# Kernel optimization log

Hardware: AMD Instinct MI355X
Metric: run time of the kernel (lower is better)

The kernel has to match this reference:

```python
import jax, jax.numpy as jnp
import numpy as np

B, L, C = 2, 4096, 1024
H, WIN = 16, 128            # num_heads, window_size (each side)
D = C // H                  # head_dim = 64


def setup_inputs() -> dict:
    key = jax.random.key(0)
    ks = jax.random.split(key, 9)
    s = 0.02
    return {
        "x": jax.random.normal(ks[0], (B, L, C), jnp.float32),
        # Linear weights stored as [in, out] (y = x @ W + b), same math as torch Linear.
        "wq": jax.random.normal(ks[1], (C, C), jnp.float32) * s,
        "bq": jnp.zeros((C,), jnp.float32),
        "wk": jax.random.normal(ks[2], (C, C), jnp.float32) * s,
        "bk": jnp.zeros((C,), jnp.float32),
        "wv": jax.random.normal(ks[3], (C, C), jnp.float32) * s,
        "bv": jnp.zeros((C,), jnp.float32),
        "wo": jax.random.normal(ks[4], (C, C), jnp.float32) * s,
        "bo": jnp.zeros((C,), jnp.float32),
    }


def reference(x, wq, bq, wk, bk, wv, bv, wo, bo):
    b, l, c = x.shape
    nb = l // WIN

    def heads(t):  # (B,L,C) -> (B,H,L,D)
        return t.reshape(b, l, H, D).transpose(0, 2, 1, 3)

    q = heads(x @ wq + bq)
    k = heads(x @ wk + bk)
    v = heads(x @ wv + bv)

    # and ARE included in the softmax, exactly as the original module does).
    kp = jnp.pad(k, ((0, 0), (0, 0), (WIN, WIN), (0, 0)))
    vp = jnp.pad(v, ((0, 0), (0, 0), (WIN, WIN), (0, 0)))

    idx = np.arange(nb)[:, None] * WIN + np.arange(3 * WIN)[None, :]  # [nb, 3W]
    kb = kp[:, :, idx]  # [B,H,nb,3W,D]
    vb = vp[:, :, idx]  # [B,H,nb,3W,D]
    qb = q.reshape(b, H, nb, WIN, D)

    scores = jnp.einsum('bhnqd,bhnkd->bhnqk', qb, kb) / float(np.sqrt(D))
    r = np.arange(WIN)[:, None]
    col = np.arange(3 * WIN)[None, :]
    band = jnp.asarray(np.abs(col - r - WIN) <= WIN)
    scores = jnp.where(band, scores, -jnp.inf)
    probs = jax.nn.softmax(scores, axis=-1)

    out = jnp.einsum('bhnqk,bhnkd->bhnqd', probs, vb)
    out = out.reshape(b, H, l, D).transpose(0, 2, 1, 3).reshape(b, l, c)
    return out @ wo + bo
```

## Files before the change

kernel.cpp:

```cpp
#include <hip/hip_runtime.h>

using short8  = __attribute__((ext_vector_type(8))) short;
using short4v = __attribute__((ext_vector_type(4))) short;
using floatx4 = __attribute__((ext_vector_type(4))) float;

#define MFMA_B16(a, b, c) __builtin_amdgcn_mfma_f32_16x16x32_bf16(a, b, c, 0, 0, 0)

__device__ __forceinline__ short f2bf(float f) {
  union { float f; unsigned u; } v; v.f = f;
  unsigned r = v.u + 0x7fffu + ((v.u >> 16) & 1u);
  return (short)(r >> 16);
}
__device__ __forceinline__ short f2bf_rtz(float f) {
  union { float f; unsigned u; } v; v.f = f;
  return (short)(v.u >> 16);
}

__device__ __forceinline__ void gload_lds16(const short* g, short* l) {
  __builtin_amdgcn_global_load_lds(
      (const __attribute__((address_space(1))) unsigned int*)g,
      (__attribute__((address_space(3))) unsigned int*)l, 16, 0, 0);
}

__global__ __launch_bounds__(256) void prep(
    const float4* __restrict__ x, short4v* __restrict__ xb,
    const float* __restrict__ w0, const float* __restrict__ w1,
    const float* __restrict__ w2, const float* __restrict__ w3,
    short* __restrict__ wT) {
  __shared__ float tile[32][33];
  int blk = blockIdx.x;
  if (blk < 8192) {
    int i = blk * 256 + threadIdx.x;
    float4 v = x[i];
    short4v o = { f2bf(v.x), f2bf(v.y), f2bf(v.z), f2bf(v.w) };
    xb[i] = o;
  } else {
    int r = blk - 8192;
    int z = r >> 10; r &= 1023;
    const float* w = z == 0 ? w0 : (z == 1 ? w1 : (z == 2 ? w2 : w3));
    short* out = wT + (size_t)z * 1024 * 1024;
    int n0 = (r & 31) * 32, k0 = (r >> 5) * 32;
    int tx = threadIdx.x & 31, ty = threadIdx.x >> 5;
#pragma unroll
    for (int i = 0; i < 4; ++i)
      tile[ty + i * 8][tx] = w[(size_t)(k0 + ty + i * 8) * 1024 + n0 + tx];
    __syncthreads();
#pragma unroll
    for (int i = 0; i < 4; ++i)
      out[(size_t)(n0 + ty + i * 8) * 1024 + k0 + tx] = f2bf(tile[tx][ty + i * 8]);
  }
}

__global__ __launch_bounds__(512, 2) void gemm_qkv(
    const short* __restrict__ xb, const short* __restrict__ wT,
    const float* __restrict__ bq, const float* __restrict__ bk,
    const float* __restrict__ bv, short* __restrict__ qkv) {
  __shared__ __align__(16) short As[2 * 16384];
  __shared__ __align__(16) short Bs[2 * 3 * 8192];

  int bid = blockIdx.x;
  int xcd = bid & 7;
  int idx = bid >> 3;
  int mb  = xcd * 4 + (idx & 3);
  int nb  = idx >> 2;
  int m0 = mb * 256, n0 = nb * 128;

  const int tid = threadIdx.x;
  const int w = tid >> 6, lane = tid & 63, quad = lane >> 4, l16 = lane & 15;
  const int wm = w >> 2, wn = w & 3;
  const int srow = tid >> 3;
  const int scol = ((tid & 7) ^ (srow & 7)) * 8;

  floatx4 zf = {0.f, 0.f, 0.f, 0.f};
  floatx4 acc[3][8][2];
#pragma unroll
  for (int z = 0; z < 3; ++z)
#pragma unroll
    for (int i = 0; i < 8; ++i) { acc[z][i][0] = zf; acc[z][i][1] = zf; }

  const short* gA = xb + (size_t)(m0 + srow) * 1024 + scol;
  const short* gB0 = wT + (size_t)(n0 + srow) * 1024 + scol;

  auto stA = [&](int buf, int q, int kt) {
    gload_lds16(gA + (size_t)q * 64 * 1024 + kt * 64,
                As + buf * 16384 + q * 4096 + w * 512);
  };
  auto stB = [&](int buf, int z, int q, int kt) {
    gload_lds16(gB0 + (size_t)z * 1024 * 1024 + (size_t)q * 64 * 1024 + kt * 64,
                Bs + (buf * 3 + z) * 8192 + q * 4096 + w * 512);
  };

  short8 aF[8], bF[4];
  auto ldA = [&](int buf, int mh) {
    const char* base = (const char*)(As + buf * 16384);
#pragma unroll
    for (int m = 0; m < 4; ++m)
#pragma unroll
      for (int kk = 0; kk < 2; ++kk) {
        int row = wm * 128 + mh * 64 + m * 16 + l16;
        int off = row * 128 + kk * 64 + quad * 16;
        off ^= (row & 7) << 4;
        aF[m * 2 + kk] = *(const short8*)(base + off);
      }
  };
  auto ldB = [&](int buf, int z) {
    const char* base = (const char*)(Bs + (buf * 3 + z) * 8192);
#pragma unroll
    for (int n = 0; n < 2; ++n)
#pragma unroll
      for (int kk = 0; kk < 2; ++kk) {
        int row = wn * 32 + n * 16 + l16;
        int off = row * 128 + kk * 64 + quad * 16;
        off ^= (row & 7) << 4;
        bF[n * 2 + kk] = *(const short8*)(base + off);
      }
  };
  auto mm = [&](int z, int mh) {
#pragma unroll
    for (int m = 0; m < 4; ++m)
#pragma unroll
      for (int n = 0; n < 2; ++n)
#pragma unroll
        for (int kk = 0; kk < 2; ++kk)
          acc[z][mh * 4 + m][n] =
              MFMA_B16(aF[m * 2 + kk], bF[n * 2 + kk], acc[z][mh * 4 + m][n]);
  };

  stA(0, 0, 0); stA(0, 1, 0); stA(0, 2, 0); stA(0, 3, 0);
  stB(0, 0, 0, 0); stB(0, 0, 1, 0); stB(0, 1, 0, 0); stB(0, 1, 1, 0);
  stB(0, 2, 0, 0); stB(0, 2, 1, 0);
  stA(1, 0, 1); stA(1, 2, 1); stA(1, 1, 1); stA(1, 3, 1);
  stB(1, 0, 0, 1); stB(1, 0, 1, 1); stB(1, 1, 0, 1); stB(1, 1, 1, 1);
  asm volatile("s_waitcnt vmcnt(8)" ::: "memory");
  __builtin_amdgcn_s_barrier();

#pragma unroll 2
  for (int t = 0; t < 16; ++t) {
    const int cb = t & 1, nbuf = cb ^ 1;
    ldA(cb, 0);
    ldB(cb, 0);
    if (t + 1 < 16) { stB(nbuf, 2, 0, t + 1); stB(nbuf, 2, 1, t + 1); }
    __builtin_amdgcn_s_setprio(1); mm(0, 0); __builtin_amdgcn_s_setprio(0);
    __builtin_amdgcn_s_barrier();
    ldB(cb, 1);
    if (t + 2 < 16) { stA(cb, 0, t + 2); stA(cb, 2, t + 2); }
    __builtin_amdgcn_s_setprio(1); mm(1, 0); __builtin_amdgcn_s_setprio(0);
    __builtin_amdgcn_s_barrier();
    ldB(cb, 2);
    __builtin_amdgcn_s_setprio(1); mm(2, 0); __builtin_amdgcn_s_setprio(0);
    __builtin_amdgcn_s_barrier();
    ldA(cb, 1);
    ldB(cb, 0);
    __builtin_amdgcn_s_setprio(1); mm(0, 1); __builtin_amdgcn_s_setprio(0);
    __builtin_amdgcn_s_barrier();
    ldB(cb, 1);
    if (t + 2 < 16) {
      stA(cb, 1, t + 2); stA(cb, 3, t + 2);
      stB(cb, 0, 0, t + 2); stB(cb, 0, 1, t + 2);
    }
    __builtin_amdgcn_s_setprio(1); mm(1, 1); __builtin_amdgcn_s_setprio(0);
    __builtin_amdgcn_s_barrier();
    ldB(cb, 2);
    if (t + 2 < 16) { stB(cb, 1, 0, t + 2); stB(cb, 1, 1, t + 2); }
    __builtin_amdgcn_s_setprio(1); mm(2, 1); __builtin_amdgcn_s_setprio(0);
    if (t + 2 < 16) {
      asm volatile("s_waitcnt vmcnt(8)" ::: "memory");
    } else {
      asm volatile("s_waitcnt vmcnt(0)" ::: "memory");
    }
    __builtin_amdgcn_s_barrier();
  }

  const float* biases[3] = {bq, bk, bv};
#pragma unroll
  for (int z = 0; z < 3; ++z) {
    const float* bias = biases[z];
    short* out = qkv + (size_t)z * 8192 * 1024;
    float qs = (z == 0) ? 0.125f * 1.44269504f : 1.0f;
#pragma unroll
    for (int mf = 0; mf < 8; ++mf)
#pragma unroll
      for (int nf = 0; nf < 2; ++nf)
#pragma unroll
        for (int rg = 0; rg < 4; ++rg) {
          int m = m0 + wm * 128 + mf * 16 + quad * 4 + rg;
          int cc = n0 + wn * 32 + nf * 16 + l16;
          float v = (acc[z][mf][nf][rg] + bias[cc]) * qs;
          int b = m >> 12, l = m & 4095;
          int hh = cc >> 6, d = cc & 63;
          out[((size_t)(b * 16 + hh) * 4096 + l) * 64 + d] = f2bf(v);
        }
  }
}

__global__ __launch_bounds__(256) void attn_kern(const short* __restrict__ qkv,
                                                 short* __restrict__ attnb) {
  const int L = 4096, H = 16;
  int n = blockIdx.x, h = blockIdx.y, b = blockIdx.z;
  const size_t hs = (size_t)L * 64;
  const short* Qp = qkv + (size_t)(b * H + h) * hs;
  const short* Kp = qkv + (size_t)8192 * 1024 + (size_t)(b * H + h) * hs;
  const short* Vp = qkv + (size_t)2 * 8192 * 1024 + (size_t)(b * H + h) * hs;

  __shared__ __align__(16) short kt[128][72];
  __shared__ __align__(16) short vt[64][136];
  __shared__ __align__(16) short pl[4][32][136];

  int tid = threadIdx.x, w = tid >> 6, lane = tid & 63, quad = lane >> 4, l16 = lane & 15;

  short8 onesf;
  {
    short ov = (l16 == 0) ? (short)0x3F80 : (short)0;
#pragma unroll
    for (int j = 0; j < 8; ++j) onesf[j] = ov;
  }

  short8 qf[2][2];
#pragma unroll
  for (int rt = 0; rt < 2; ++rt)
#pragma unroll
    for (int ks = 0; ks < 2; ++ks)
      qf[rt][ks] = *(const short8*)(Qp + (size_t)(n * 128 + w * 32 + rt * 16 + l16) * 64 + ks * 32 + quad * 8);

  floatx4 zf = {0.f, 0.f, 0.f, 0.f};
  floatx4 o[2][4];
  floatx4 osum[2];
#pragma unroll
  for (int i = 0; i < 2; ++i) {
    osum[i] = zf;
#pragma unroll
    for (int j = 0; j < 4; ++j) o[i][j] = zf;
  }

#pragma unroll
  for (int c = 0; c < 3; ++c) {
    int bk = n - 1 + c;
    bool inr = (c == 1) || (c == 0 ? (n > 0) : (n < 31));
    __syncthreads();
    if (inr) {
      const short* kc_ = Kp + (size_t)bk * 128 * 64;
      int kr = tid >> 2, ksg = (tid & 3) * 16;
#pragma unroll
      for (int p = 0; p < 2; ++p) {
        int r2 = p * 64 + kr;
        *(short8*)(&kt[r2][ksg])     = *(const short8*)(kc_ + r2 * 64 + ksg);
        *(short8*)(&kt[r2][ksg + 8]) = *(const short8*)(kc_ + r2 * 64 + ksg + 8);
      }
      const short* vc_ = Vp + (size_t)bk * 128 * 64;
      int vkey = tid & 31, vsg = (tid >> 5) * 8;
#pragma unroll
      for (int p = 0; p < 4; ++p) {
        int r2 = p * 32 + vkey;
        short8 vv = *(const short8*)(vc_ + r2 * 64 + vsg);
#pragma unroll
        for (int j = 0; j < 8; ++j) vt[vsg + j][r2] = vv[j];
      }
    } else {
      short8 z8 = {0, 0, 0, 0, 0, 0, 0, 0};
      int kr = tid >> 2, ksg = (tid & 3) * 16;
#pragma unroll
      for (int p = 0; p < 2; ++p) {
        int r2 = p * 64 + kr;
        *(short8*)(&kt[r2][ksg])     = z8;
        *(short8*)(&kt[r2][ksg + 8]) = z8;
      }
      int vr = tid >> 2, vsg2 = (tid & 3) * 32;
#pragma unroll
      for (int q2 = 0; q2 < 4; ++q2) *(short8*)(&vt[vr][vsg2 + q2 * 8]) = z8;
    }
    __syncthreads();

    floatx4 s[2][8];
#pragma unroll
    for (int rt = 0; rt < 2; ++rt)
#pragma unroll
      for (int ct = 0; ct < 8; ++ct) s[rt][ct] = zf;
#pragma unroll
    for (int ct = 0; ct < 8; ++ct) {
      bool any = (c == 0) ? (ct >= w * 2) : (c == 2) ? (ct <= w * 2 + 1) : true;
      if (any) {
        short8 kf0 = *(const short8*)(&kt[ct * 16 + l16][quad * 8]);
        short8 kf1 = *(const short8*)(&kt[ct * 16 + l16][32 + quad * 8]);
#pragma unroll
        for (int rt = 0; rt < 2; ++rt) {
          bool valid = (c == 0) ? (ct >= w * 2 + rt) : (c == 2) ? (ct <= w * 2 + rt) : true;
          if (valid) {
            s[rt][ct] = MFMA_B16(qf[rt][0], kf0, s[rt][ct]);
            s[rt][ct] = MFMA_B16(qf[rt][1], kf1, s[rt][ct]);
          }
        }
      }
    }

#pragma unroll
    for (int rt = 0; rt < 2; ++rt) {
      int wrt = w * 2 + rt;
#pragma unroll
      for (int ct = 0; ct < 8; ++ct) {
        bool tileMasked = (c == 0) ? (ct < wrt) : (c == 2) ? (ct > wrt) : false;
        bool ksDead = (c == 0) ? (2 * (ct >> 1) + 1 < wrt)
                    : (c == 2) ? (2 * (ct >> 1) > wrt) : false;
        bool diag = (c != 1) && (ct == wrt);
        if (ksDead) continue;
        if (tileMasked) {
#pragma unroll
          for (int rg = 0; rg < 4; ++rg)
            pl[w][rt * 16 + quad * 4 + rg][ct * 16 + l16] = 0;
        } else if (diag) {
#pragma unroll
          for (int rg = 0; rg < 4; ++rg) {
            int r16 = quad * 4 + rg;
            float p = exp2f(s[rt][ct][rg]);
            if (c == 0) p = (l16 < r16) ? 0.f : p;
            else        p = (l16 > r16) ? 0.f : p;
            pl[w][rt * 16 + r16][ct * 16 + l16] = f2bf_rtz(p);
          }
        } else {
#pragma unroll
          for (int rg = 0; rg < 4; ++rg)
            pl[w][rt * 16 + quad * 4 + rg][ct * 16 + l16] = f2bf_rtz(exp2f(s[rt][ct][rg]));
        }
      }
    }

    __syncthreads();

#pragma unroll
    for (int ks = 0; ks < 4; ++ks) {
      bool anyrt = (c == 0) ? (2 * ks + 1 >= w * 2) : (c == 2) ? (2 * ks <= w * 2 + 1) : true;
      if (!anyrt) continue;
      short8 vf[4];
#pragma unroll
      for (int ct = 0; ct < 4; ++ct)
        vf[ct] = *(const short8*)(&vt[ct * 16 + l16][ks * 32 + quad * 8]);
#pragma unroll
      for (int rt = 0; rt < 2; ++rt) {
        int wrt = w * 2 + rt;
        bool ksDead = (c == 0) ? (2 * ks + 1 < wrt) : (c == 2) ? (2 * ks > wrt) : false;
        if (ksDead) continue;
        short8 pf = *(const short8*)(&pl[w][rt * 16 + l16][ks * 32 + quad * 8]);
#pragma unroll
        for (int ct = 0; ct < 4; ++ct) o[rt][ct] = MFMA_B16(pf, vf[ct], o[rt][ct]);
        osum[rt] = MFMA_B16(pf, onesf, osum[rt]);
      }
    }
  }

#pragma unroll
  for (int rt = 0; rt < 2; ++rt) {
#pragma unroll
    for (int rg = 0; rg < 4; ++rg) {
      float ssum = __shfl(osum[rt][rg], lane & 48);
      float inv = 1.f / ssum;
      int r = n * 128 + w * 32 + rt * 16 + quad * 4 + rg;
#pragma unroll
      for (int ct = 0; ct < 4; ++ct)
        attnb[(size_t)(b * L + r) * 1024 + h * 64 + ct * 16 + l16] =
            f2bf(o[rt][ct][rg] * inv);
    }
  }
}

__global__ __launch_bounds__(512, 2) void gemm_out(
    const short* __restrict__ attnb, const short* __restrict__ wTo,
    const float* __restrict__ bo, float* __restrict__ outp) {
  __shared__ __align__(16) short As[2 * 8192];
  __shared__ __align__(16) short Bs[2 * 16384];

  int bid = blockIdx.x;
  int xcd = bid & 7;
  int idx = bid >> 3;
  int mb  = xcd * 8 + (idx & 7);
  int nb  = idx >> 3;
  int m0 = mb * 128, n0 = nb * 256;

  const int tid = threadIdx.x;
  const int w = tid >> 6, lane = tid & 63, quad = lane >> 4, l16 = lane & 15;
  const int wm = w >> 2, wn = w & 3;
  const int srow = tid >> 3;
  const int scol = ((tid & 7) ^ (srow & 7)) * 8;

  floatx4 zf = {0.f, 0.f, 0.f, 0.f};
  floatx4 acc[4][4];
#pragma unroll
  for (int i = 0; i < 4; ++i)
#pragma unroll
    for (int j = 0; j < 4; ++j) acc[i][j] = zf;

  const short* gA = attnb + (size_t)(m0 + srow) * 1024 + scol;
  const short* gB = wTo + (size_t)(n0 + srow) * 1024 + scol;

  auto stA = [&](int buf, int q, int kt) {
    gload_lds16(gA + (size_t)q * 64 * 1024 + kt * 64,
                As + buf * 8192 + q * 4096 + w * 512);
  };
  auto stB = [&](int buf, int q, int kt) {
    gload_lds16(gB + (size_t)q * 64 * 1024 + kt * 64,
                Bs + buf * 16384 + q * 4096 + w * 512);
  };

  short8 aF[8], bF[4];
  auto ldA = [&](int buf) {
    const char* base = (const char*)(As + buf * 8192);
#pragma unroll
    for (int m = 0; m < 4; ++m)
#pragma unroll
      for (int kk = 0; kk < 2; ++kk) {
        int row = wm * 64 + m * 16 + l16;
        int off = row * 128 + kk * 64 + quad * 16;
        off ^= (row & 7) << 4;
        aF[m * 2 + kk] = *(const short8*)(base + off);
      }
  };
  auto ldB = [&](int buf, int nh) {
    const char* base = (const char*)(Bs + buf * 16384);
#pragma unroll
    for (int n = 0; n < 2; ++n)
#pragma unroll
      for (int kk = 0; kk < 2; ++kk) {
        int row = wn * 64 + nh * 32 + n * 16 + l16;
        int off = row * 128 + kk * 64 + quad * 16;
        off ^= (row & 7) << 4;
        bF[n * 2 + kk] = *(const short8*)(base + off);
      }
  };
  auto mm = [&](int nh) {
#pragma unroll
    for (int m = 0; m < 4; ++m)
#pragma unroll
      for (int n = 0; n < 2; ++n)
#pragma unroll
        for (int kk = 0; kk < 2; ++kk)
          acc[m][nh * 2 + n] =
              MFMA_B16(aF[m * 2 + kk], bF[n * 2 + kk], acc[m][nh * 2 + n]);
  };

  stA(0, 0, 0); stA(0, 1, 0);
  stB(0, 0, 0); stB(0, 1, 0); stB(0, 2, 0); stB(0, 3, 0);
  stA(1, 0, 1); stA(1, 1, 1);
  asm volatile("s_waitcnt vmcnt(2)" ::: "memory");
  __builtin_amdgcn_s_barrier();

#pragma unroll 2
  for (int t = 0; t < 16; ++t) {
    const int cb = t & 1, nbuf = cb ^ 1;
    ldA(cb);
    ldB(cb, 0);
    if (t + 1 < 16) {
      stB(nbuf, 0, t + 1); stB(nbuf, 1, t + 1);
      stB(nbuf, 2, t + 1); stB(nbuf, 3, t + 1);
    }
    __builtin_amdgcn_s_setprio(1); mm(0); __builtin_amdgcn_s_setprio(0);
    __builtin_amdgcn_s_barrier();
    ldB(cb, 1);
    if (t + 2 < 16) { stA(cb, 0, t + 2); stA(cb, 1, t + 2); }
    __builtin_amdgcn_s_setprio(1); mm(1); __builtin_amdgcn_s_setprio(0);
    if (t + 2 < 16) {
      asm volatile("s_waitcnt vmcnt(2)" ::: "memory");
    } else {
      asm volatile("s_waitcnt vmcnt(0)" ::: "memory");
    }
    __builtin_amdgcn_s_barrier();
  }

#pragma unroll
  for (int mf = 0; mf < 4; ++mf)
#pragma unroll
    for (int nf = 0; nf < 4; ++nf)
#pragma unroll
      for (int rg = 0; rg < 4; ++rg) {
        int m = m0 + wm * 64 + mf * 16 + quad * 4 + rg;
        int cc = n0 + wn * 64 + nf * 16 + l16;
        outp[(size_t)m * 1024 + cc] = acc[mf][nf][rg] + bo[cc];
      }
}

extern "C" void kernel_launch(void* const* d_in, const int* in_sizes, int n_in,
                              void* d_out, int out_size, void* d_ws, size_t ws_size,
                              hipStream_t stream) {
  const float* x  = (const float*)d_in[0];
  const float* wq = (const float*)d_in[1];
  const float* bq = (const float*)d_in[2];
  const float* wk = (const float*)d_in[3];
  const float* bk = (const float*)d_in[4];
  const float* wv = (const float*)d_in[5];
  const float* bv = (const float*)d_in[6];
  const float* wo = (const float*)d_in[7];
  const float* bo = (const float*)d_in[8];

  char* ws = (char*)d_ws;
  short* xb    = (short*)ws;
  short* wT    = (short*)(ws + (16u << 20));
  short* qkv   = (short*)(ws + (24u << 20));
  short* attnb = (short*)(ws + (72u << 20));

  prep<<<12288, 256, 0, stream>>>((const float4*)x, (short4v*)xb, wq, wk, wv, wo, wT);
  gemm_qkv<<<256, 512, 0, stream>>>(xb, wT, bq, bk, bv, qkv);
  attn_kern<<<dim3(32, 16, 2), 256, 0, stream>>>(qkv, attnb);
  gemm_out<<<256, 512, 0, stream>>>(attnb, wT + 3u * 1024 * 1024, bo, (float*)d_out);
}
```

Measured before the change: 241.9 us.

## Retile QKV GEMM to one projection per block with 256x256 tiles

```diff
diff --git a/kernel.cpp b/kernel.cpp
--- a/kernel.cpp
+++ b/kernel.cpp
@@ -56,14 +56,18 @@
     const float* __restrict__ bq, const float* __restrict__ bk,
     const float* __restrict__ bv, short* __restrict__ qkv) {
   __shared__ __align__(16) short As[2 * 16384];
-  __shared__ __align__(16) short Bs[2 * 3 * 8192];
-
+  __shared__ __align__(16) short Bs[2 * 16384];
   int bid = blockIdx.x;
   int xcd = bid & 7;
   int idx = bid >> 3;
-  int mb  = xcd * 4 + (idx & 3);
-  int nb  = idx >> 2;
-  int m0 = mb * 256, n0 = nb * 128;
+  int z   = idx >> 4;
+  int r   = idx & 15;
+  int mb  = xcd * 4 + (r & 3);
+  int nb  = r >> 2;
+  const short* wt = wT + (size_t)z * 1024 * 1024;
+  const float* bias = z == 0 ? bq : (z == 1 ? bk : bv);
+  short* out = qkv + (size_t)z * 8192 * 1024;
+  int m0 = mb * 256, n0 = nb * 256;
 
   const int tid = threadIdx.x;
   const int w = tid >> 6, lane = tid & 63, quad = lane >> 4, l16 = lane & 15;
@@ -72,26 +76,26 @@
   const int scol = ((tid & 7) ^ (srow & 7)) * 8;
 
   floatx4 zf = {0.f, 0.f, 0.f, 0.f};
-  floatx4 acc[3][8][2];
-#pragma unroll
-  for (int z = 0; z < 3; ++z)
-#pragma unroll
-    for (int i = 0; i < 8; ++i) { acc[z][i][0] = zf; acc[z][i][1] = zf; }
+  floatx4 acc[8][4];
+#pragma unroll
+  for (int i = 0; i < 8; ++i)
+#pragma unroll
+    for (int j = 0; j < 4; ++j) acc[i][j] = zf;
 
   const short* gA = xb + (size_t)(m0 + srow) * 1024 + scol;
-  const short* gB0 = wT + (size_t)(n0 + srow) * 1024 + scol;
+  const short* gB = wt + (size_t)(n0 + srow) * 1024 + scol;
 
   auto stA = [&](int buf, int q, int kt) {
     gload_lds16(gA + (size_t)q * 64 * 1024 + kt * 64,
                 As + buf * 16384 + q * 4096 + w * 512);
   };
-  auto stB = [&](int buf, int z, int q, int kt) {
-    gload_lds16(gB0 + (size_t)z * 1024 * 1024 + (size_t)q * 64 * 1024 + kt * 64,
-                Bs + (buf * 3 + z) * 8192 + q * 4096 + w * 512);
-  };
-
-  short8 aF[8], bF[4];
-  auto ldA = [&](int buf, int mh) {
+  auto stB = [&](int buf, int q, int kt) {
+    gload_lds16(gB + (size_t)q * 64 * 1024 + kt * 64,
+                Bs + buf * 16384 + q * 4096 + w * 512);
+  };
+
+  short8 aF0[8], aF1[8], bF0[4], bF1[4];
+  auto ldA = [&](int buf, int mh, short8* dst) {
     const char* base = (const char*)(As + buf * 16384);
 #pragma unroll
     for (int m = 0; m < 4; ++m)
@@ -100,97 +104,82 @@
         int row = wm * 128 + mh * 64 + m * 16 + l16;
         int off = row * 128 + kk * 64 + quad * 16;
         off ^= (row & 7) << 4;
-        aF[m * 2 + kk] = *(const short8*)(base + off);
-      }
-  };
-  auto ldB = [&](int buf, int z) {
-    const char* base = (const char*)(Bs + (buf * 3 + z) * 8192);
+        dst[m * 2 + kk] = *(const short8*)(base + off);
+      }
+  };
+  auto ldB = [&](int buf, int nh, short8* dst) {
+    const char* base = (const char*)(Bs + buf * 16384);
 #pragma unroll
     for (int n = 0; n < 2; ++n)
 #pragma unroll
       for (int kk = 0; kk < 2; ++kk) {
-        int row = wn * 32 + n * 16 + l16;
+        int row = wn * 64 + nh * 32 + n * 16 + l16;
         int off = row * 128 + kk * 64 + quad * 16;
         off ^= (row & 7) << 4;
-        bF[n * 2 + kk] = *(const short8*)(base + off);
-      }
-  };
-  auto mm = [&](int z, int mh) {
+        dst[n * 2 + kk] = *(const short8*)(base + off);
+      }
+  };
+  auto mm = [&](const short8* a, const short8* b, int mh, int nh) {
 #pragma unroll
     for (int m = 0; m < 4; ++m)
 #pragma unroll
       for (int n = 0; n < 2; ++n)
 #pragma unroll
         for (int kk = 0; kk < 2; ++kk)
-          acc[z][mh * 4 + m][n] =
-              MFMA_B16(aF[m * 2 + kk], bF[n * 2 + kk], acc[z][mh * 4 + m][n]);
+          acc[mh * 4 + m][nh * 2 + n] =
+              MFMA_B16(a[m * 2 + kk], b[n * 2 + kk], acc[mh * 4 + m][nh * 2 + n]);
   };
 
   stA(0, 0, 0); stA(0, 1, 0); stA(0, 2, 0); stA(0, 3, 0);
-  stB(0, 0, 0, 0); stB(0, 0, 1, 0); stB(0, 1, 0, 0); stB(0, 1, 1, 0);
-  stB(0, 2, 0, 0); stB(0, 2, 1, 0);
-  stA(1, 0, 1); stA(1, 2, 1); stA(1, 1, 1); stA(1, 3, 1);
-  stB(1, 0, 0, 1); stB(1, 0, 1, 1); stB(1, 1, 0, 1); stB(1, 1, 1, 1);
+  stB(0, 0, 0); stB(0, 1, 0); stB(0, 2, 0); stB(0, 3, 0);
+  stA(1, 0, 1); stA(1, 1, 1); stA(1, 2, 1); stA(1, 3, 1);
+  stB(1, 0, 1); stB(1, 1, 1); stB(1, 2, 1); stB(1, 3, 1);
   asm volatile("s_waitcnt vmcnt(8)" ::: "memory");
   __builtin_amdgcn_s_barrier();
 
 #pragma unroll 2
   for (int t = 0; t < 16; ++t) {
-    const int cb = t & 1, nbuf = cb ^ 1;
-    ldA(cb, 0);
-    ldB(cb, 0);
-    if (t + 1 < 16) { stB(nbuf, 2, 0, t + 1); stB(nbuf, 2, 1, t + 1); }
-    __builtin_amdgcn_s_setprio(1); mm(0, 0); __builtin_amdgcn_s_setprio(0);
-    __builtin_amdgcn_s_barrier();
-    ldB(cb, 1);
+    const int cb = t & 1;
+    ldA(cb, 0, aF0);
+    ldB(cb, 0, bF0);
+    ldB(cb, 1, bF1);
+    __builtin_amdgcn_s_setprio(1); mm(aF0, bF0, 0, 0); __builtin_amdgcn_s_setprio(0);
+    __builtin_amdgcn_s_barrier();
+    ldA(cb, 1, aF1);
     if (t + 2 < 16) { stA(cb, 0, t + 2); stA(cb, 2, t + 2); }
-    __builtin_amdgcn_s_setprio(1); mm(1, 0); __builtin_amdgcn_s_setprio(0);
-    __builtin_amdgcn_s_barrier();
-    ldB(cb, 2);
-    __builtin_amdgcn_s_setprio(1); mm(2, 0); __builtin_amdgcn_s_setprio(0);
-    __builtin_amdgcn_s_barrier();
-    ldA(cb, 1);
-    ldB(cb, 0);
-    __builtin_amdgcn_s_setprio(1); mm(0, 1); __builtin_amdgcn_s_setprio(0);
-    __builtin_amdgcn_s_barrier();
-    ldB(cb, 1);
+    __builtin_amdgcn_s_setprio(1); mm(aF0, bF1, 0, 1); __builtin_amdgcn_s_setprio(0);
+    __builtin_amdgcn_s_barrier();
+    if (t + 2 < 16) {
+      stB(cb, 0, t + 2); stB(cb, 1, t + 2);
+      stB(cb, 2, t + 2); stB(cb, 3, t + 2);
+    }
+    __builtin_amdgcn_s_setprio(1); mm(aF1, bF0, 1, 0); __builtin_amdgcn_s_setprio(0);
+    __builtin_amdgcn_s_barrier();
     if (t + 2 < 16) {
       stA(cb, 1, t + 2); stA(cb, 3, t + 2);
-      stB(cb, 0, 0, t + 2); stB(cb, 0, 1, t + 2);
-    }
-    __builtin_amdgcn_s_setprio(1); mm(1, 1); __builtin_amdgcn_s_setprio(0);
-    __builtin_amdgcn_s_barrier();
-    ldB(cb, 2);
-    if (t + 2 < 16) { stB(cb, 1, 0, t + 2); stB(cb, 1, 1, t + 2); }
-    __builtin_amdgcn_s_setprio(1); mm(2, 1); __builtin_amdgcn_s_setprio(0);
-    if (t + 2 < 16) {
+      __builtin_amdgcn_s_setprio(1); mm(aF1, bF1, 1, 1); __builtin_amdgcn_s_setprio(0);
       asm volatile("s_waitcnt vmcnt(8)" ::: "memory");
     } else {
+      __builtin_amdgcn_s_setprio(1); mm(aF1, bF1, 1, 1); __builtin_amdgcn_s_setprio(0);
       asm volatile("s_waitcnt vmcnt(0)" ::: "memory");
     }
     __builtin_amdgcn_s_barrier();
   }
 
-  const float* biases[3] = {bq, bk, bv};
-#pragma unroll
-  for (int z = 0; z < 3; ++z) {
-    const float* bias = biases[z];
-    short* out = qkv + (size_t)z * 8192 * 1024;
-    float qs = (z == 0) ? 0.125f * 1.44269504f : 1.0f;
-#pragma unroll
-    for (int mf = 0; mf < 8; ++mf)
-#pragma unroll
-      for (int nf = 0; nf < 2; ++nf)
-#pragma unroll
-        for (int rg = 0; rg < 4; ++rg) {
-          int m = m0 + wm * 128 + mf * 16 + quad * 4 + rg;
-          int cc = n0 + wn * 32 + nf * 16 + l16;
-          float v = (acc[z][mf][nf][rg] + bias[cc]) * qs;
-          int b = m >> 12, l = m & 4095;
-          int hh = cc >> 6, d = cc & 63;
-          out[((size_t)(b * 16 + hh) * 4096 + l) * 64 + d] = f2bf(v);
-        }
-  }
+  float qs = (z == 0) ? 0.125f * 1.44269504f : 1.0f;
+#pragma unroll
+  for (int mf = 0; mf < 8; ++mf)
+#pragma unroll
+    for (int nf = 0; nf < 4; ++nf)
+#pragma unroll
+      for (int rg = 0; rg < 4; ++rg) {
+        int m = m0 + wm * 128 + mf * 16 + quad * 4 + rg;
+        int cc = n0 + wn * 64 + nf * 16 + l16;
+        float v = (acc[mf][nf][rg] + bias[cc]) * qs;
+        int b = m >> 12, l = m & 4095;
+        int hh = cc >> 6, d = cc & 63;
+        out[((size_t)(b * 16 + hh) * 4096 + l) * 64 + d] = f2bf(v);
+      }
 }
 
 __global__ __launch_bounds__(256) void attn_kern(const short* __restrict__ qkv,
@@ -495,7 +484,7 @@
   short* attnb = (short*)(ws + (72u << 20));
 
   prep<<<12288, 256, 0, stream>>>((const float4*)x, (short4v*)xb, wq, wk, wv, wo, wT);
-  gemm_qkv<<<256, 512, 0, stream>>>(xb, wT, bq, bk, bv, qkv);
+  gemm_qkv<<<384, 512, 0, stream>>>(xb, wT, bq, bk, bv, qkv);
   attn_kern<<<dim3(32, 16, 2), 256, 0, stream>>>(qkv, attnb);
   gemm_out<<<256, 512, 0, stream>>>(attnb, wT + 3u * 1024 * 1024, bo, (float*)d_out);
 }
```

New measurement: 285.0 us. +17.8%, slower.
